# Kernel tuning notes

Measured on AMD Instinct MI355X. Metric: run time of the kernel, lower is better.

The kernel has to match this reference:

```python
import jax, jax.numpy as jnp
import numpy as np

B, T, E, U, V = 32, 128, 512, 1024, 50000


def setup_inputs() -> dict:
    key = jax.random.key(0)
    ks = jax.random.split(key, 10)
    s = lambda fan: 1.0 / np.sqrt(fan)
    return {
        "tokens": jax.random.randint(ks[0], (B, T), 0, V, dtype=jnp.int32),
        "emb":  jax.random.normal(ks[1], (V, E), dtype=jnp.float32) * 0.02,
        "W0":   jax.random.normal(ks[2], (E, 4 * U), dtype=jnp.float32) * s(E),
        "U0":   jax.random.normal(ks[3], (U, 4 * U), dtype=jnp.float32) * s(U),
        "b0":   jnp.zeros((4 * U,), dtype=jnp.float32),
        "W1":   jax.random.normal(ks[4], (U, 4 * U), dtype=jnp.float32) * s(U),
        "U1":   jax.random.normal(ks[5], (U, 4 * U), dtype=jnp.float32) * s(U),
        "b1":   jnp.zeros((4 * U,), dtype=jnp.float32),
        "fc_w": jax.random.normal(ks[6], (U, 1), dtype=jnp.float32) * s(U),
        "fc_b": jnp.zeros((1,), dtype=jnp.float32),
    }


def _lstm_cell(xt, state, W, Uh, b):
    # Keras LSTMCell gate order: i, f, g(candidate), o
    h, c = state
    z = xt @ W + h @ Uh + b  # [B, 4U]
    i, f, g, o = jnp.split(z, 4, axis=-1)
    c_new = jax.nn.sigmoid(f) * c + jax.nn.sigmoid(i) * jnp.tanh(g)
    h_new = jax.nn.sigmoid(o) * jnp.tanh(c_new)
    return h_new, (h_new, c_new)


def reference(tokens, emb, W0, U0, b0, W1, U1, b1, fc_w, fc_b):
    x = emb[tokens]                      # [B, T, E]
    xs = jnp.transpose(x, (1, 0, 2))     # [T, B, E] for scan over time

    # Faithful to original: after each step `h0 = h1`, so both cells read the
    # SAME previous state (layer-1's). Carry is a single (h, c) pair.
    init = (jnp.zeros((B, U), x.dtype), jnp.zeros((B, U), x.dtype))

    def step(carry, xt):
        out0, _s0 = _lstm_cell(xt, carry, W0, U0, b0)
        out1, s1 = _lstm_cell(out0, carry, W1, U1, b1)
        return s1, None

    (h_last, _c_last), _ = jax.lax.scan(step, init, xs)
    logits = h_last @ fc_w + fc_b        # [B, 1]
    return jax.nn.sigmoid(logits)
```

## Files before the change

### kernel.cpp

```cpp
#include <hip/hip_runtime.h>
#include <math.h>

#define BB 32
#define TT 128
#define EE 512
#define UU 1024
#define GG 4096
#define HP 36

typedef float f32x4 __attribute__((ext_vector_type(4)));

__device__ __forceinline__ float sigmoidf_(float x){ return 1.0f/(1.0f + expf(-x)); }

__global__ void gather_k(const int* __restrict__ tokens, const float* __restrict__ emb,
                         float* __restrict__ xT){
  int idx = blockIdx.x*256 + threadIdx.x;
  int b = idx & 31, e = (idx>>5)&511, t = idx>>14;
  int tok = tokens[b*TT + t];
  xT[idx] = emb[(size_t)tok*EE + e];
}

__global__ __launch_bounds__(512) void lstm_k2(
    const float* __restrict__ xTt,
    const float* __restrict__ W0,
    const float* __restrict__ U0,
    const float* __restrict__ U1,
    const float* __restrict__ b0,
    const float* __restrict__ hT,
    const float* __restrict__ cT,
    float* __restrict__ h0T,
    float* __restrict__ zp)
{
  __shared__ float hs[256*HP];
  __shared__ float red[8][512];
  __shared__ float zbuf[32*17];
  int tid = threadIdx.x;
  int bid = blockIdx.x;
  int ub = bid*4;
  int cq = tid & 3, bq = (tid>>2)&7, kq = tid>>5;
  int col = cq*UU + ub;
  float acc [4][4] = {{0}};
  float acc2[4][4] = {{0}};

  for (int ch = 0; ch < EE; ch += 256) {
    __syncthreads();
    const f32x4* s4 = (const f32x4*)(xTt + ch*BB);
    for (int i = tid; i < 2048; i += 512) {
      int r = i>>3, c4 = i&7;
      *(f32x4*)&hs[r*HP + c4*4] = s4[i];
    }
    __syncthreads();
    int kb = kq*16;
    #pragma unroll 2
    for (int kk=0; kk<16; kk+=4){
      int k = kb + kk;
      int kg = ch + k;
      f32x4 w[4], hv[4];
      #pragma unroll
      for (int j=0;j<4;++j) w[j] = *(const f32x4*)(W0 + (size_t)(kg+j)*GG + col);
      #pragma unroll
      for (int j=0;j<4;++j) hv[j] = *(const f32x4*)&hs[(k+j)*HP + bq*4];
      #pragma unroll
      for (int j=0;j<4;++j)
        #pragma unroll
        for (int bi=0;bi<4;++bi)
          #pragma unroll
          for (int ci=0;ci<4;++ci)
            acc[bi][ci] += hv[j][bi]*w[j][ci];
    }
  }

  for (int ch = 0; ch < UU; ch += 256) {
    __syncthreads();
    const f32x4* s4 = (const f32x4*)(hT + ch*BB);
    for (int i = tid; i < 2048; i += 512) {
      int r = i>>3, c4 = i&7;
      *(f32x4*)&hs[r*HP + c4*4] = s4[i];
    }
    __syncthreads();
    int kb = kq*16;
    #pragma unroll 2
    for (int kk=0; kk<16; kk+=4){
      int k = kb + kk;
      int kg = ch + k;
      f32x4 w[4], w2[4], hv[4];
      #pragma unroll
      for (int j=0;j<4;++j) w[j]  = *(const f32x4*)(U0 + (size_t)(kg+j)*GG + col);
      #pragma unroll
      for (int j=0;j<4;++j) w2[j] = *(const f32x4*)(U1 + (size_t)(kg+j)*GG + col);
      #pragma unroll
      for (int j=0;j<4;++j) hv[j] = *(const f32x4*)&hs[(k+j)*HP + bq*4];
      #pragma unroll
      for (int j=0;j<4;++j)
        #pragma unroll
        for (int bi=0;bi<4;++bi)
          #pragma unroll
          for (int ci=0;ci<4;++ci){
            acc [bi][ci] += hv[j][bi]*w [j][ci];
            acc2[bi][ci] += hv[j][bi]*w2[j][ci];
          }
    }
  }

  #pragma unroll
  for (int bi=0;bi<4;++bi)
    #pragma unroll
    for (int ci=0;ci<4;++ci){
      acc [bi][ci] += __shfl_xor(acc [bi][ci], 32, 64);
      acc2[bi][ci] += __shfl_xor(acc2[bi][ci], 32, 64);
    }

  if ((tid & 32) == 0){
    #pragma unroll
    for (int bi=0;bi<4;++bi){
      int out = (bq*4+bi)*16 + cq*4;
      f32x4 v = {acc[bi][0],acc[bi][1],acc[bi][2],acc[bi][3]};
      *(f32x4*)&red[kq>>1][out] = v;
    }
  }
  __syncthreads();
  {
    int o = tid;
    if (o < 512){
      float s = 0.f;
      #pragma unroll
      for (int q=0;q<8;++q) s += red[q][o];
      zbuf[(o>>4)*17 + (o&15)] = s;
    }
  }
  __syncthreads();
  if ((tid & 32) == 0){
    #pragma unroll
    for (int bi=0;bi<4;++bi){
      int out = (bq*4+bi)*16 + cq*4;
      f32x4 v = {acc2[bi][0],acc2[bi][1],acc2[bi][2],acc2[bi][3]};
      *(f32x4*)&red[kq>>1][out] = v;
    }
  }
  __syncthreads();
  if (tid < 128){
    int b = tid>>2, uj = tid&3;
    int u = ub + uj;
    float zi = zbuf[b*17 + 0 + uj] + b0[0*UU + u];
    float zf = zbuf[b*17 + 4 + uj] + b0[1*UU + u];
    float zg = zbuf[b*17 + 8 + uj] + b0[2*UU + u];
    float zo = zbuf[b*17 +12 + uj] + b0[3*UU + u];
    float c0 = sigmoidf_(zf)*cT[u*BB + b] + sigmoidf_(zi)*tanhf(zg);
    h0T[u*BB + b] = sigmoidf_(zo)*tanhf(c0);
  }
  {
    int o = tid;
    if (o < 512){
      float s = 0.f;
      #pragma unroll
      for (int q=0;q<8;++q) s += red[q][o];
      zp[bid*512 + o] = s;
    }
  }
}

__global__ __launch_bounds__(512) void lstm_k3(
    const float* __restrict__ h0T,
    const float* __restrict__ W1,
    const float* __restrict__ b1,
    const float* __restrict__ zp,
    float* __restrict__ hT,
    float* __restrict__ cT)
{
  __shared__ float hs[256*HP];
  __shared__ float red[8][512];
  __shared__ float zbuf[32*17];
  int tid = threadIdx.x, bid = blockIdx.x, ub = bid*4;
  int cq = tid&3, bq = (tid>>2)&7, kq = tid>>5;
  int col = cq*UU + ub;
  float acc[4][4] = {{0}};

  for (int ch=0; ch<UU; ch+=256){
    __syncthreads();
    const f32x4* s4 = (const f32x4*)(h0T + ch*BB);
    for (int i=tid;i<2048;i+=512){ int r=i>>3,c4=i&7; *(f32x4*)&hs[r*HP+c4*4]=s4[i]; }
    __syncthreads();
    int kb = kq*16;
    #pragma unroll 2
    for (int kk=0;kk<16;kk+=4){
      int k = kb+kk, kg = ch+k;
      f32x4 w[4], hv[4];
      #pragma unroll
      for (int j=0;j<4;++j) w[j] = *(const f32x4*)(W1 + (size_t)(kg+j)*GG + col);
      #pragma unroll
      for (int j=0;j<4;++j) hv[j] = *(const f32x4*)&hs[(k+j)*HP + bq*4];
      #pragma unroll
      for (int j=0;j<4;++j)
        #pragma unroll
        for (int bi=0;bi<4;++bi)
          #pragma unroll
          for (int ci=0;ci<4;++ci)
            acc[bi][ci] += hv[j][bi]*w[j][ci];
    }
  }

  #pragma unroll
  for (int bi=0;bi<4;++bi)
    #pragma unroll
    for (int ci=0;ci<4;++ci)
      acc[bi][ci] += __shfl_xor(acc[bi][ci], 32, 64);

  if ((tid & 32) == 0){
    #pragma unroll
    for (int bi=0;bi<4;++bi){
      int out = (bq*4+bi)*16 + cq*4;
      f32x4 v = {acc[bi][0],acc[bi][1],acc[bi][2],acc[bi][3]};
      *(f32x4*)&red[kq>>1][out] = v;
    }
  }
  __syncthreads();
  {
    int o = tid;
    if (o < 512){
      float s = 0.f;
      #pragma unroll
      for (int q=0;q<8;++q) s += red[q][o];
      zbuf[(o>>4)*17 + (o&15)] = s;
    }
  }
  __syncthreads();
  if (tid < 128){
    int b = tid>>2, uj = tid&3;
    int u = ub + uj;
    const float* zpb = zp + bid*512 + b*16;
    float zi = zbuf[b*17 + 0 + uj] + zpb[ 0+uj] + b1[0*UU + u];
    float zf = zbuf[b*17 + 4 + uj] + zpb[ 4+uj] + b1[1*UU + u];
    float zg = zbuf[b*17 + 8 + uj] + zpb[ 8+uj] + b1[2*UU + u];
    float zo = zbuf[b*17 +12 + uj] + zpb[12+uj] + b1[3*UU + u];
    float cold = cT[u*BB + b];
    float cn = sigmoidf_(zf)*cold + sigmoidf_(zi)*tanhf(zg);
    float hn = sigmoidf_(zo)*tanhf(cn);
    hT[u*BB + b] = hn;
    cT[u*BB + b] = cn;
  }
}

__global__ __launch_bounds__(256) void lstm_out(const float* __restrict__ hT,
    const float* __restrict__ fcw, const float* __restrict__ fcb, float* __restrict__ out){
  __shared__ float r[256];
  int b = blockIdx.x, tid = threadIdx.x;
  float s = 0.f;
  for (int u = tid; u < UU; u += 256) s += hT[u*BB + b] * fcw[u];
  r[tid] = s; __syncthreads();
  for (int st=128; st>0; st>>=1){ if (tid<st) r[tid]+=r[tid+st]; __syncthreads(); }
  if (tid==0) out[b] = 1.0f/(1.0f+expf(-(r[0]+fcb[0])));
}

extern "C" void kernel_launch(void* const* d_in, const int* in_sizes, int n_in,
                              void* d_out, int out_size, void* d_ws, size_t ws_size,
                              hipStream_t stream) {
  const int*   tokens = (const int*)  d_in[0];
  const float* emb    = (const float*)d_in[1];
  const float* W0     = (const float*)d_in[2];
  const float* U0     = (const float*)d_in[3];
  const float* b0     = (const float*)d_in[4];
  const float* W1     = (const float*)d_in[5];
  const float* U1     = (const float*)d_in[6];
  const float* b1     = (const float*)d_in[7];
  const float* fcw    = (const float*)d_in[8];
  const float* fcb    = (const float*)d_in[9];

  float* ws  = (float*)d_ws;
  float* xT  = ws;
  float* hT  = xT  + (size_t)TT*EE*BB;
  float* cT  = hT  + 32768;
  float* h0T = cT  + 32768;
  float* zp  = h0T + 32768;

  hipMemsetAsync(hT, 0, (size_t)2*32768*sizeof(float), stream);

  gather_k<<<8192, 256, 0, stream>>>(tokens, emb, xT);

  for (int t = 0; t < TT; ++t) {
    lstm_k2<<<256, 512, 0, stream>>>(xT + (size_t)t*EE*BB, W0, U0, U1, b0, hT, cT, h0T, zp);
    lstm_k3<<<256, 512, 0, stream>>>(h0T, W1, b1, zp, hT, cT);
  }
  lstm_out<<<32, 256, 0, stream>>>(hT, fcw, fcb, (float*)d_out);
}
```

Before: 11.52 ms.

## Rebalance LSTM step kernels: move U1 GEMV into k3, drop LDS staging

The recurrent U1 product moves from the first step kernel into the second, which now reads the previous h from a ping-pong buffer. This removes the zp partial-sum round trip and balances the weight streaming between the two kernels. Both kernels drop LDS staging of activations and read them straight from global/L2. They reduce over k with wave shuffles instead of a shared-memory tree, and blocks are remapped in a swizzled order. The kernels now depend on cache hits for the broadcast activation reads, and some __syncthreads calls without a clear purpose remain.

```diff
diff --git a/kernel.cpp b/kernel.cpp
--- a/kernel.cpp
+++ b/kernel.cpp
@@ -6,11 +6,10 @@
 #define EE 512
 #define UU 1024
 #define GG 4096
-#define HP 36
 
 typedef float f32x4 __attribute__((ext_vector_type(4)));
 
-__device__ __forceinline__ float sigmoidf_(float x){ return 1.0f/(1.0f + expf(-x)); }
+__device__ __forceinline__ float sigf(float x){ return 1.0f/(1.0f + expf(-x)); }
 
 __global__ void gather_k(const int* __restrict__ tokens, const float* __restrict__ emb,
                          float* __restrict__ xT){
@@ -20,223 +19,149 @@
   xT[idx] = emb[(size_t)tok*EE + e];
 }
 
+
 __global__ __launch_bounds__(512) void lstm_k2(
     const float* __restrict__ xTt,
     const float* __restrict__ W0,
     const float* __restrict__ U0,
-    const float* __restrict__ U1,
     const float* __restrict__ b0,
-    const float* __restrict__ hT,
+    const float* __restrict__ hin,
     const float* __restrict__ cT,
-    float* __restrict__ h0T,
-    float* __restrict__ zp)
+    float* __restrict__ h0T)
 {
-  __shared__ float hs[256*HP];
-  __shared__ float red[8][512];
-  __shared__ float zbuf[32*17];
+  __shared__ float zb[16*36];
   int tid = threadIdx.x;
-  int bid = blockIdx.x;
-  int ub = bid*4;
-  int cq = tid & 3, bq = (tid>>2)&7, kq = tid>>5;
-  int col = cq*UU + ub;
-  float acc [4][4] = {{0}};
-  float acc2[4][4] = {{0}};
-
-  for (int ch = 0; ch < EE; ch += 256) {
-    __syncthreads();
-    const f32x4* s4 = (const f32x4*)(xTt + ch*BB);
-    for (int i = tid; i < 2048; i += 512) {
-      int r = i>>3, c4 = i&7;
-      *(f32x4*)&hs[r*HP + c4*4] = s4[i];
-    }
-    __syncthreads();
-    int kb = kq*16;
-    #pragma unroll 2
-    for (int kk=0; kk<16; kk+=4){
-      int k = kb + kk;
-      int kg = ch + k;
-      f32x4 w[4], hv[4];
+  int lb  = ((blockIdx.x & 7) << 5) | (blockIdx.x >> 3);
+  int ub  = lb << 2;
+  int kq = tid & 15, cq = (tid >> 4) & 3, bq = tid >> 6;
+  int bq4 = bq << 2;
+  int col = cq * UU + ub;
+  float acc[4][4] = {{0.f,0.f,0.f,0.f},{0.f,0.f,0.f,0.f},{0.f,0.f,0.f,0.f},{0.f,0.f,0.f,0.f}};
+
+  {
+    const float* wp = W0 + col;
+    #pragma unroll 4
+    for (int j = 0; j < 32; ++j) {
+      int k = (j << 4) + kq;
+      f32x4 w  = *(const f32x4*)(wp + (size_t)k * GG);
+      f32x4 xv = *(const f32x4*)(xTt + (k << 5) + bq4);
       #pragma unroll
-      for (int j=0;j<4;++j) w[j] = *(const f32x4*)(W0 + (size_t)(kg+j)*GG + col);
-      #pragma unroll
-      for (int j=0;j<4;++j) hv[j] = *(const f32x4*)&hs[(k+j)*HP + bq*4];
-      #pragma unroll
-      for (int j=0;j<4;++j)
+      for (int bi = 0; bi < 4; ++bi)
         #pragma unroll
-        for (int bi=0;bi<4;++bi)
-          #pragma unroll
-          for (int ci=0;ci<4;++ci)
-            acc[bi][ci] += hv[j][bi]*w[j][ci];
-    }
-  }
-
-  for (int ch = 0; ch < UU; ch += 256) {
-    __syncthreads();
-    const f32x4* s4 = (const f32x4*)(hT + ch*BB);
-    for (int i = tid; i < 2048; i += 512) {
-      int r = i>>3, c4 = i&7;
-      *(f32x4*)&hs[r*HP + c4*4] = s4[i];
-    }
-    __syncthreads();
-    int kb = kq*16;
-    #pragma unroll 2
-    for (int kk=0; kk<16; kk+=4){
-      int k = kb + kk;
-      int kg = ch + k;
-      f32x4 w[4], w2[4], hv[4];
-      #pragma unroll
-      for (int j=0;j<4;++j) w[j]  = *(const f32x4*)(U0 + (size_t)(kg+j)*GG + col);
-      #pragma unroll
-      for (int j=0;j<4;++j) w2[j] = *(const f32x4*)(U1 + (size_t)(kg+j)*GG + col);
-      #pragma unroll
-      for (int j=0;j<4;++j) hv[j] = *(const f32x4*)&hs[(k+j)*HP + bq*4];
-      #pragma unroll
-      for (int j=0;j<4;++j)
-        #pragma unroll
-        for (int bi=0;bi<4;++bi)
-          #pragma unroll
-          for (int ci=0;ci<4;++ci){
-            acc [bi][ci] += hv[j][bi]*w [j][ci];
-            acc2[bi][ci] += hv[j][bi]*w2[j][ci];
-          }
-    }
-  }
-
-  #pragma unroll
-  for (int bi=0;bi<4;++bi)
-    #pragma unroll
-    for (int ci=0;ci<4;++ci){
-      acc [bi][ci] += __shfl_xor(acc [bi][ci], 32, 64);
-      acc2[bi][ci] += __shfl_xor(acc2[bi][ci], 32, 64);
-    }
-
-  if ((tid & 32) == 0){
-    #pragma unroll
-    for (int bi=0;bi<4;++bi){
-      int out = (bq*4+bi)*16 + cq*4;
-      f32x4 v = {acc[bi][0],acc[bi][1],acc[bi][2],acc[bi][3]};
-      *(f32x4*)&red[kq>>1][out] = v;
+        for (int ci = 0; ci < 4; ++ci)
+          acc[bi][ci] += xv[bi] * w[ci];
     }
   }
   __syncthreads();
   {
-    int o = tid;
-    if (o < 512){
-      float s = 0.f;
-      #pragma unroll
-      for (int q=0;q<8;++q) s += red[q][o];
-      zbuf[(o>>4)*17 + (o&15)] = s;
-    }
-  }
+    const float* wp = U0 + col;
+    for (int jb = 0; jb < 64; jb += 32) {
+      #pragma unroll 4
+      for (int j = jb; j < jb + 32; ++j) {
+        int k = (j << 4) + kq;
+        f32x4 w  = *(const f32x4*)(wp + (size_t)k * GG);
+        f32x4 hv = *(const f32x4*)(hin + (k << 5) + bq4);
+        #pragma unroll
+        for (int bi = 0; bi < 4; ++bi)
+          #pragma unroll
+          for (int ci = 0; ci < 4; ++ci)
+            acc[bi][ci] += hv[bi] * w[ci];
+      }
+      __syncthreads();
+    }
+  }
+  #pragma unroll
+  for (int bi = 0; bi < 4; ++bi)
+    #pragma unroll
+    for (int ci = 0; ci < 4; ++ci) {
+      float a = acc[bi][ci];
+      a += __shfl_xor(a, 1); a += __shfl_xor(a, 2);
+      a += __shfl_xor(a, 4); a += __shfl_xor(a, 8);
+      acc[bi][ci] = a;
+    }
+  #pragma unroll
+  for (int ci = 0; ci < 4; ++ci)
+    if (kq == ci) {
+      f32x4 z = {acc[0][ci], acc[1][ci], acc[2][ci], acc[3][ci]};
+      *(f32x4*)&zb[(cq*4 + ci)*36 + bq4] = z;
+    }
   __syncthreads();
-  if ((tid & 32) == 0){
-    #pragma unroll
-    for (int bi=0;bi<4;++bi){
-      int out = (bq*4+bi)*16 + cq*4;
-      f32x4 v = {acc2[bi][0],acc2[bi][1],acc2[bi][2],acc2[bi][3]};
-      *(f32x4*)&red[kq>>1][out] = v;
-    }
-  }
-  __syncthreads();
-  if (tid < 128){
-    int b = tid>>2, uj = tid&3;
+  if (tid < 128) {
+    int b = tid & 31, uj = tid >> 5;
     int u = ub + uj;
-    float zi = zbuf[b*17 + 0 + uj] + b0[0*UU + u];
-    float zf = zbuf[b*17 + 4 + uj] + b0[1*UU + u];
-    float zg = zbuf[b*17 + 8 + uj] + b0[2*UU + u];
-    float zo = zbuf[b*17 +12 + uj] + b0[3*UU + u];
-    float c0 = sigmoidf_(zf)*cT[u*BB + b] + sigmoidf_(zi)*tanhf(zg);
-    h0T[u*BB + b] = sigmoidf_(zo)*tanhf(c0);
-  }
-  {
-    int o = tid;
-    if (o < 512){
-      float s = 0.f;
-      #pragma unroll
-      for (int q=0;q<8;++q) s += red[q][o];
-      zp[bid*512 + o] = s;
-    }
+    float zi = zb[(0*4 + uj)*36 + b] + b0[u];
+    float zf = zb[(1*4 + uj)*36 + b] + b0[UU + u];
+    float zg = zb[(2*4 + uj)*36 + b] + b0[2*UU + u];
+    float zo = zb[(3*4 + uj)*36 + b] + b0[3*UU + u];
+    float c0 = sigf(zf) * cT[(u<<5) + b] + sigf(zi) * tanhf(zg);
+    h0T[(u<<5) + b] = sigf(zo) * tanhf(c0);
   }
 }
 
 __global__ __launch_bounds__(512) void lstm_k3(
     const float* __restrict__ h0T,
     const float* __restrict__ W1,
+    const float* __restrict__ U1,
     const float* __restrict__ b1,
-    const float* __restrict__ zp,
-    float* __restrict__ hT,
+    const float* __restrict__ hin,
+    float* __restrict__ hout,
     float* __restrict__ cT)
 {
-  __shared__ float hs[256*HP];
-  __shared__ float red[8][512];
-  __shared__ float zbuf[32*17];
-  int tid = threadIdx.x, bid = blockIdx.x, ub = bid*4;
-  int cq = tid&3, bq = (tid>>2)&7, kq = tid>>5;
-  int col = cq*UU + ub;
-  float acc[4][4] = {{0}};
-
-  for (int ch=0; ch<UU; ch+=256){
+  __shared__ float zb[16*36];
+  int tid = threadIdx.x;
+  int lb  = ((blockIdx.x & 7) << 5) | (blockIdx.x >> 3);
+  int ub  = lb << 2;
+  int kq = tid & 15, cq = (tid >> 4) & 3, bq = tid >> 6;
+  int bq4 = bq << 2;
+  int col = cq * UU + ub;
+  float acc[4][4] = {{0.f,0.f,0.f,0.f},{0.f,0.f,0.f,0.f},{0.f,0.f,0.f,0.f},{0.f,0.f,0.f,0.f}};
+
+  const float* w1p = W1 + col;
+  const float* u1p = U1 + col;
+  for (int jb = 0; jb < 64; jb += 32) {
+    #pragma unroll 4
+    for (int j = jb; j < jb + 32; ++j) {
+      int k = (j << 4) + kq;
+      f32x4 wa = *(const f32x4*)(w1p + (size_t)k * GG);
+      f32x4 wb = *(const f32x4*)(u1p + (size_t)k * GG);
+      f32x4 ha = *(const f32x4*)(h0T + (k << 5) + bq4);
+      f32x4 hb = *(const f32x4*)(hin + (k << 5) + bq4);
+      #pragma unroll
+      for (int bi = 0; bi < 4; ++bi)
+        #pragma unroll
+        for (int ci = 0; ci < 4; ++ci)
+          acc[bi][ci] += ha[bi] * wa[ci] + hb[bi] * wb[ci];
+    }
     __syncthreads();
-    const f32x4* s4 = (const f32x4*)(h0T + ch*BB);
-    for (int i=tid;i<2048;i+=512){ int r=i>>3,c4=i&7; *(f32x4*)&hs[r*HP+c4*4]=s4[i]; }
-    __syncthreads();
-    int kb = kq*16;
-    #pragma unroll 2
-    for (int kk=0;kk<16;kk+=4){
-      int k = kb+kk, kg = ch+k;
-      f32x4 w[4], hv[4];
-      #pragma unroll
-      for (int j=0;j<4;++j) w[j] = *(const f32x4*)(W1 + (size_t)(kg+j)*GG + col);
-      #pragma unroll
-      for (int j=0;j<4;++j) hv[j] = *(const f32x4*)&hs[(k+j)*HP + bq*4];
-      #pragma unroll
-      for (int j=0;j<4;++j)
-        #pragma unroll
-        for (int bi=0;bi<4;++bi)
-          #pragma unroll
-          for (int ci=0;ci<4;++ci)
-            acc[bi][ci] += hv[j][bi]*w[j][ci];
-    }
-  }
-
-  #pragma unroll
-  for (int bi=0;bi<4;++bi)
+  }
+  #pragma unroll
+  for (int bi = 0; bi < 4; ++bi)
     #pragma unroll
-    for (int ci=0;ci<4;++ci)
-      acc[bi][ci] += __shfl_xor(acc[bi][ci], 32, 64);
-
-  if ((tid & 32) == 0){
-    #pragma unroll
-    for (int bi=0;bi<4;++bi){
-      int out = (bq*4+bi)*16 + cq*4;
-      f32x4 v = {acc[bi][0],acc[bi][1],acc[bi][2],acc[bi][3]};
-      *(f32x4*)&red[kq>>1][out] = v;
-    }
-  }
+    for (int ci = 0; ci < 4; ++ci) {
+      float a = acc[bi][ci];
+      a += __shfl_xor(a, 1); a += __shfl_xor(a, 2);
+      a += __shfl_xor(a, 4); a += __shfl_xor(a, 8);
+      acc[bi][ci] = a;
+    }
+  #pragma unroll
+  for (int ci = 0; ci < 4; ++ci)
+    if (kq == ci) {
+      f32x4 z = {acc[0][ci], acc[1][ci], acc[2][ci], acc[3][ci]};
+      *(f32x4*)&zb[(cq*4 + ci)*36 + bq4] = z;
+    }
   __syncthreads();
-  {
-    int o = tid;
-    if (o < 512){
-      float s = 0.f;
-      #pragma unroll
-      for (int q=0;q<8;++q) s += red[q][o];
-      zbuf[(o>>4)*17 + (o&15)] = s;
-    }
-  }
-  __syncthreads();
-  if (tid < 128){
-    int b = tid>>2, uj = tid&3;
+  if (tid < 128) {
+    int b = tid & 31, uj = tid >> 5;
     int u = ub + uj;
-    const float* zpb = zp + bid*512 + b*16;
-    float zi = zbuf[b*17 + 0 + uj] + zpb[ 0+uj] + b1[0*UU + u];
-    float zf = zbuf[b*17 + 4 + uj] + zpb[ 4+uj] + b1[1*UU + u];
-    float zg = zbuf[b*17 + 8 + uj] + zpb[ 8+uj] + b1[2*UU + u];
-    float zo = zbuf[b*17 +12 + uj] + zpb[12+uj] + b1[3*UU + u];
-    float cold = cT[u*BB + b];
-    float cn = sigmoidf_(zf)*cold + sigmoidf_(zi)*tanhf(zg);
-    float hn = sigmoidf_(zo)*tanhf(cn);
-    hT[u*BB + b] = hn;
-    cT[u*BB + b] = cn;
+    float zi = zb[(0*4 + uj)*36 + b] + b1[u];
+    float zf = zb[(1*4 + uj)*36 + b] + b1[UU + u];
+    float zg = zb[(2*4 + uj)*36 + b] + b1[2*UU + u];
+    float zo = zb[(3*4 + uj)*36 + b] + b1[3*UU + u];
+    float cold = cT[(u<<5) + b];
+    float cn = sigf(zf) * cold + sigf(zi) * tanhf(zg);
+    float hn = sigf(zo) * tanhf(cn);
+    hout[(u<<5) + b] = hn;
+    cT[(u<<5) + b] = cn;
   }
 }
 
@@ -245,10 +170,10 @@
   __shared__ float r[256];
   int b = blockIdx.x, tid = threadIdx.x;
   float s = 0.f;
-  for (int u = tid; u < UU; u += 256) s += hT[u*BB + b] * fcw[u];
+  for (int u = tid; u < UU; u += 256) s += hT[(u<<5) + b] * fcw[u];
   r[tid] = s; __syncthreads();
-  for (int st=128; st>0; st>>=1){ if (tid<st) r[tid]+=r[tid+st]; __syncthreads(); }
-  if (tid==0) out[b] = 1.0f/(1.0f+expf(-(r[0]+fcb[0])));
+  for (int st = 128; st > 0; st >>= 1){ if (tid < st) r[tid] += r[tid+st]; __syncthreads(); }
+  if (tid == 0) out[b] = 1.0f/(1.0f + expf(-(r[0] + fcb[0])));
 }
 
 extern "C" void kernel_launch(void* const* d_in, const int* in_sizes, int n_in,
@@ -267,18 +192,20 @@
 
   float* ws  = (float*)d_ws;
   float* xT  = ws;
-  float* hT  = xT  + (size_t)TT*EE*BB;
-  float* cT  = hT  + 32768;
-  float* h0T = cT  + 32768;
-  float* zp  = h0T + 32768;
-
-  hipMemsetAsync(hT, 0, (size_t)2*32768*sizeof(float), stream);
+  float* hA  = xT  + (size_t)TT*EE*BB;
+  float* cT  = hA  + 32768;
+  float* hB  = cT  + 32768;
+  float* h0T = hB  + 32768;
+
+  hipMemsetAsync(hA, 0, (size_t)2*32768*sizeof(float), stream);
 
   gather_k<<<8192, 256, 0, stream>>>(tokens, emb, xT);
 
   for (int t = 0; t < TT; ++t) {
-    lstm_k2<<<256, 512, 0, stream>>>(xT + (size_t)t*EE*BB, W0, U0, U1, b0, hT, cT, h0T, zp);
-    lstm_k3<<<256, 512, 0, stream>>>(h0T, W1, b1, zp, hT, cT);
-  }
-  lstm_out<<<32, 256, 0, stream>>>(hT, fcw, fcb, (float*)d_out);
-}
+    const float* hin  = (t & 1) ? hB : hA;
+    float*       hout = (t & 1) ? hA : hB;
+    lstm_k2<<<256, 512, 0, stream>>>(xT + (size_t)t*EE*BB, W0, U0, b0, hin, cT, h0T);
+    lstm_k3<<<256, 512, 0, stream>>>(h0T, W1, U1, b1, hin, hout, cT);
+  }
+  lstm_out<<<32, 256, 0, stream>>>(hA, fcw, fcb, (float*)d_out);
+}
```

New measurement: 18.68 ms. +62.1%, slower.
